# Kernel tuning notes

Measured on AMD Instinct MI355X. Metric: run time of the kernel, lower is better.

Reference implementation:

```python
import jax, jax.numpy as jnp
import numpy as np

B, N, M, C = 1024, 2048, 128, 512
EPS = 1e-8


def setup_inputs() -> dict:
    key = jax.random.key(0)
    k1, k2, k3, k4, k5 = jax.random.split(key, 5)
    x = jax.random.normal(k1, (B, C), dtype=jnp.float32)
    u = jax.random.uniform(k2, (B, N), dtype=jnp.float32) + 1e-3
    w_prev = u / jnp.sum(u, axis=1, keepdims=True)  # valid attention distribution
    mem = jax.random.normal(k3, (B, N, M), dtype=jnp.float32)
    # xavier-uniform-ish fc_read weight (gain 1.4), tiny-std bias
    limit = 1.4 * np.sqrt(6.0 / (C + (M + 6)))
    W = jax.random.uniform(k4, (M + 6, C), dtype=jnp.float32, minval=-limit, maxval=limit)
    b = 0.01 * jax.random.normal(k5, (M + 6,), dtype=jnp.float32)
    return {"x": x, "w_prev": w_prev, "mem": mem, "W": W, "b": b}


def reference(x, w_prev, mem, W, b):
    m = mem.shape[-1]
    o = x @ W.T + b                                   # [B, M+6]
    k = o[:, :m]                                      # key [B, M]
    beta = jax.nn.softplus(o[:, m:m + 1])             # [B, 1]
    g = jax.nn.sigmoid(o[:, m + 1:m + 2])             # [B, 1]
    s = jax.nn.softmax(o[:, m + 2:m + 5], axis=1)     # [B, 3] shift weights
    gamma = 1.0 + jax.nn.softplus(o[:, m + 5:m + 6])  # [B, 1]

    # content addressing: cosine similarity, beta-sharpened softmax
    dot = jnp.einsum('bnm,bm->bn', mem, k)
    denom = jnp.linalg.norm(mem, axis=-1) * jnp.linalg.norm(k, axis=-1, keepdims=True) + EPS
    w_c = jax.nn.softmax(beta * (dot / denom), axis=1)  # [B, N]

    # gate interpolation
    w_g = g * w_c + (1.0 - g) * w_prev

    # circular convolution with 3-tap shift: w_t[i] = sum_j s[j] * w_g[(i+j-1) mod N]
    w_t = (s[:, 0:1] * jnp.roll(w_g, 1, axis=1)
           + s[:, 1:2] * w_g
           + s[:, 2:3] * jnp.roll(w_g, -1, axis=1))

    # sharpening
    w_pow = w_t ** gamma
    w = w_pow / (jnp.sum(w_pow, axis=1, keepdims=True) + 1e-16)

    # weighted read
    r = jnp.einsum('bn,bnm->bm', w, mem)
    return (r, w)
```

## Files before the change

kernel.cpp:

```cpp
#include <hip/hip_runtime.h>
#include <math.h>

#define B 1024
#define N 2048
#define M 128
#define C 512
#define OD (M + 6)
#define EPSF 1e-8f
#define CHUNK 512
#define NCHUNK 4
#define NGRP 64
#define ITERS (B / NGRP)
#define GRID_F (NCHUNK * NGRP)
#define AGENT __HIP_MEMORY_SCOPE_AGENT

__device__ __forceinline__ float softplusf(float x) {
    return fmaxf(x, 0.f) + log1pf(expf(-fabsf(x)));
}
__device__ __forceinline__ float sigmoidf_(float x) {
    return 1.f / (1.f + expf(-x));
}

__device__ __forceinline__ void bar_lds() {
    asm volatile("s_waitcnt lgkmcnt(0)" ::: "memory");
    __builtin_amdgcn_s_barrier();
}

__global__ __launch_bounds__(256) void k_head(
    const float* __restrict__ x, const float* __restrict__ W,
    const float* __restrict__ bias, float* __restrict__ kbuf,
    float* __restrict__ params)
{
    const int b = blockIdx.x;
    __shared__ float xs[C];
    __shared__ float os[OD];
    __shared__ float red[128];

    for (int i = threadIdx.x; i < C; i += 256) xs[i] = x[(size_t)b * C + i];
    __syncthreads();

    if (threadIdx.x < OD) {
        const int j = threadIdx.x;
        const float4* wr = (const float4*)(W + (size_t)j * C);
        float acc = 0.f;
#pragma unroll 8
        for (int c = 0; c < C / 4; ++c) {
            float4 wv = wr[c];
            acc = fmaf(wv.x, xs[4 * c + 0], acc);
            acc = fmaf(wv.y, xs[4 * c + 1], acc);
            acc = fmaf(wv.z, xs[4 * c + 2], acc);
            acc = fmaf(wv.w, xs[4 * c + 3], acc);
        }
        os[j] = acc + bias[j];
    }
    __syncthreads();

    if (threadIdx.x < M) {
        float v = os[threadIdx.x];
        kbuf[(size_t)b * M + threadIdx.x] = v;
        red[threadIdx.x] = v * v;
    }
    __syncthreads();
    for (int s = 64; s > 0; s >>= 1) {
        if (threadIdx.x < s) red[threadIdx.x] += red[threadIdx.x + s];
        __syncthreads();
    }
    if (threadIdx.x == 0) {
        float kn = sqrtf(red[0]);
        float beta = softplusf(os[M]);
        float g = sigmoidf_(os[M + 1]);
        float a0 = os[M + 2], a1 = os[M + 3], a2 = os[M + 4];
        float mx = fmaxf(a0, fmaxf(a1, a2));
        float e0 = expf(a0 - mx), e1 = expf(a1 - mx), e2 = expf(a2 - mx);
        float inv = 1.f / (e0 + e1 + e2);
        float gamma = 1.f + softplusf(os[M + 5]);
        float* p = params + (size_t)b * 8;
        p[0] = beta; p[1] = g; p[2] = e0 * inv; p[3] = e1 * inv;
        p[4] = e2 * inv; p[5] = gamma; p[6] = kn; p[7] = 0.f;
    }
}

__global__ __launch_bounds__(1024, 4) void k_fused(
    const float* __restrict__ mem, const float* __restrict__ kbuf,
    const float* __restrict__ params, const float* __restrict__ w_prev,
    float* __restrict__ w_out,
    float* __restrict__ sPart, float* __restrict__ tPart,
    int* __restrict__ cnt1, float* __restrict__ edgeE,
    float* __restrict__ rpart)
{
    __shared__ float2 redT[CHUNK * 33];
    __shared__ float eA[CHUNK];
    __shared__ float wgA[CHUNK + 2];
    __shared__ float pwA[CHUNK];
    __shared__ float redA[16 * 128];
    __shared__ float partS[16];
    __shared__ float partT[8];
    __shared__ float bcast[4];

    const int tid  = threadIdx.x;
    const int lane = tid & 63;
    const int wv   = tid >> 6;
    const int half = lane >> 5;
    const int l32  = lane & 31;
    const int hw   = wv * 2 + half;

    const int cid  = blockIdx.x >> 6;
    const int bgrp = blockIdx.x & 63;

    for (int it = 0; it < ITERS; ++it) {
        const int b = bgrp * ITERS + it;
        const float* cb = mem + ((size_t)b * N + cid * CHUNK) * M;

        float4 frag[16];
#pragma unroll
        for (int j = 0; j < 16; ++j)
            frag[j] = ((const float4*)(cb + (size_t)(hw * 16 + j) * M))[l32];

        float wp_t = 0.f, wpL = 0.f, wpR = 0.f;
        if (tid < CHUNK)
            wp_t = w_prev[(size_t)b * N + cid * CHUNK + tid];
        if (tid == 0) {
            wpL = w_prev[(size_t)b * N + ((cid * CHUNK + N - 1) & (N - 1))];
            wpR = w_prev[(size_t)b * N + ((cid * CHUNK + CHUNK) & (N - 1))];
        }
        const float4 kv = ((const float4*)(kbuf + (size_t)b * M))[l32];
        const float4 p0 = ((const float4*)(params + (size_t)b * 8))[0];
        const float4 p1 = ((const float4*)(params + (size_t)b * 8))[1];
        const float beta = p0.x, kn = p1.z;

#pragma unroll
        for (int j = 0; j < 16; ++j) {
            const float4 f = frag[j];
            const float dot = f.x * kv.x + f.y * kv.y + f.z * kv.z + f.w * kv.w;
            const float sq  = f.x * f.x + f.y * f.y + f.z * f.z + f.w * f.w;
            redT[(hw * 16 + j) * 33 + l32] = make_float2(dot, sq);
        }
        bar_lds();

        {
            const int r = tid >> 1, q = tid & 1;
            const float2* rowp = &redT[r * 33 + q * 16];
            float dot = 0.f, sq = 0.f;
#pragma unroll
            for (int g = 0; g < 16; ++g) { dot += rowp[g].x; sq += rowp[g].y; }
            dot += __shfl_xor(dot, 1, 64);
            sq  += __shfl_xor(sq,  1, 64);
            float e = 0.f;
            if (q == 0) {
                const float z = beta * dot / (sqrtf(sq) * kn + EPSF);
                e = expf(z);
                eA[r] = e;
            }
            float myS = e;
#pragma unroll
            for (int s = 1; s <= 32; s <<= 1) myS += __shfl_xor(myS, s, 64);
            if (lane == 0) partS[wv] = myS;
        }
        bar_lds();

        if (tid == 0) {
            float S = 0.f;
#pragma unroll
            for (int h = 0; h < 16; ++h) S += partS[h];
            __hip_atomic_store(&sPart[(size_t)b * NCHUNK + cid], S, __ATOMIC_RELAXED, AGENT);
            __hip_atomic_store(&edgeE[((size_t)b * NCHUNK + cid) * 2 + 0], eA[0], __ATOMIC_RELAXED, AGENT);
            __hip_atomic_store(&edgeE[((size_t)b * NCHUNK + cid) * 2 + 1], eA[CHUNK - 1], __ATOMIC_RELAXED, AGENT);
            asm volatile("s_waitcnt vmcnt(0)" ::: "memory");
            __hip_atomic_fetch_add(&cnt1[b], 1, __ATOMIC_RELAXED, AGENT);
            int tries = 0;
            while (__hip_atomic_load(&cnt1[b], __ATOMIC_RELAXED, AGENT) < NCHUNK) {
                __builtin_amdgcn_s_sleep(1);
                if (++tries > (1 << 22)) break;
            }
            float St = 0.f;
#pragma unroll
            for (int c2 = 0; c2 < NCHUNK; ++c2)
                St += __hip_atomic_load(&sPart[(size_t)b * NCHUNK + c2], __ATOMIC_RELAXED, AGENT);
            bcast[0] = 1.f / St;
            bcast[1] = __hip_atomic_load(&edgeE[((size_t)b * NCHUNK + ((cid + NCHUNK - 1) & (NCHUNK - 1))) * 2 + 1], __ATOMIC_RELAXED, AGENT);
            bcast[2] = __hip_atomic_load(&edgeE[((size_t)b * NCHUNK + ((cid + 1) & (NCHUNK - 1))) * 2 + 0], __ATOMIC_RELAXED, AGENT);
        }
        bar_lds();

        const float invS = bcast[0], eL = bcast[1], eR = bcast[2];
        const float g = p0.y, s0p = p0.z, s1p = p0.w, s2p = p1.x, gamma = p1.y;
        if (tid < CHUNK)
            wgA[tid + 1] = g * eA[tid] * invS + (1.f - g) * wp_t;
        if (tid == 0) {
            wgA[0]         = g * eL * invS + (1.f - g) * wpL;
            wgA[CHUNK + 1] = g * eR * invS + (1.f - g) * wpR;
        }
        bar_lds();

        float myT = 0.f;
        if (tid < CHUNK) {
            const float wt = s0p * wgA[tid] + s1p * wgA[tid + 1] + s2p * wgA[tid + 2];
            const float pw = powf(wt, gamma);
            pwA[tid] = pw;
            myT = pw;
        }
#pragma unroll
        for (int s = 32; s >= 1; s >>= 1) myT += __shfl_xor(myT, s, 64);
        if (lane == 0 && wv < 8) partT[wv] = myT;
        bar_lds();

        if (tid == 0) {
            float T = 0.f;
#pragma unroll
            for (int w2 = 0; w2 < 8; ++w2) T += partT[w2];
            tPart[(size_t)b * NCHUNK + cid] = T;
        }

        float4 pwv[4];
#pragma unroll
        for (int q4 = 0; q4 < 4; ++q4)
            pwv[q4] = ((const float4*)&pwA[hw * 16])[q4];
        float4 acc = make_float4(0.f, 0.f, 0.f, 0.f);
#pragma unroll
        for (int j = 0; j < 16; ++j) {
            const float pw = ((const float*)&pwv[j >> 2])[j & 3];
            acc.x = fmaf(pw, frag[j].x, acc.x);
            acc.y = fmaf(pw, frag[j].y, acc.y);
            acc.z = fmaf(pw, frag[j].z, acc.z);
            acc.w = fmaf(pw, frag[j].w, acc.w);
        }
        acc.x += __shfl_xor(acc.x, 32, 64);
        acc.y += __shfl_xor(acc.y, 32, 64);
        acc.z += __shfl_xor(acc.z, 32, 64);
        acc.w += __shfl_xor(acc.w, 32, 64);
        if (half == 0) *(float4*)&redA[wv * 128 + l32 * 4] = acc;
        bar_lds();

        if (tid < 128) {
            float s = 0.f;
#pragma unroll
            for (int w2 = 0; w2 < 16; ++w2) s += redA[w2 * 128 + tid];
            rpart[((size_t)b * NCHUNK + cid) * 128 + tid] = s;
        }
        if (tid < CHUNK)
            w_out[(size_t)b * N + cid * CHUNK + tid] = pwA[tid];
        bar_lds();
    }
}

__global__ __launch_bounds__(256) void k_norm(
    const float* __restrict__ tPart, const float* __restrict__ rpart,
    float* __restrict__ w_out, float* __restrict__ r_out)
{
    const int b = blockIdx.x, tid = threadIdx.x;
    float T = 0.f;
#pragma unroll
    for (int c = 0; c < NCHUNK; ++c) T += tPart[(size_t)b * NCHUNK + c];
    const float invT = 1.f / (T + 1e-16f);

    float4* w4 = (float4*)(w_out + (size_t)b * N);
#pragma unroll
    for (int k = 0; k < 2; ++k) {
        float4 v = w4[tid + k * 256];
        v.x *= invT; v.y *= invT; v.z *= invT; v.w *= invT;
        w4[tid + k * 256] = v;
    }
    if (tid < 128) {
        float s = 0.f;
#pragma unroll
        for (int c = 0; c < NCHUNK; ++c)
            s += rpart[((size_t)b * NCHUNK + c) * 128 + tid];
        r_out[(size_t)b * M + tid] = s * invT;
    }
}

extern "C" void kernel_launch(void* const* d_in, const int* in_sizes, int n_in,
                              void* d_out, int out_size, void* d_ws, size_t ws_size,
                              hipStream_t stream) {
    const float* x      = (const float*)d_in[0];
    const float* w_prev = (const float*)d_in[1];
    const float* mem    = (const float*)d_in[2];
    const float* W      = (const float*)d_in[3];
    const float* bias   = (const float*)d_in[4];

    float* r_out = (float*)d_out;
    float* w_out = (float*)d_out + (size_t)B * M;

    float* ws     = (float*)d_ws;
    float* kbuf   = ws;
    float* params = kbuf + (size_t)B * M;
    float* sPart  = params + (size_t)B * 8;
    float* tPart  = sPart + (size_t)B * NCHUNK;
    int*   cnt1   = (int*)(tPart + (size_t)B * NCHUNK);
    float* edgeE  = (float*)(cnt1 + B);
    float* rpart  = edgeE + (size_t)B * NCHUNK * 2;

    hipMemsetAsync(cnt1, 0, B * sizeof(int), stream);

    k_head<<<B, 256, 0, stream>>>(x, W, bias, kbuf, params);
    k_fused<<<GRID_F, 1024, 0, stream>>>(mem, kbuf, params, w_prev, w_out,
                                         sPart, tPart, cnt1, edgeE, rpart);
    k_norm<<<B, 256, 0, stream>>>(tPart, rpart, w_out, r_out);
}
```

Before: 299.4 us.

## Halve chunk size to double fused blocks and raise occupancy

Splits each batch row's N dimension into 8 chunks of 256 instead of 4 of 512, doubling the fused grid and halving the per-thread memory fragment registers. The launch bound is raised so two 1024-thread blocks can share a CU, keeping more loads in flight for this bandwidth-bound read of mem. The first reduction now pre-combines across half-waves with shuffles, which shrinks the LDS transpose buffer. The cost is more cross-block spin synchronisation per row (8 participants) and the requirement that all 512 blocks be co-resident, which a register spill or LDS overflow would break.

After: 348.6 us. +16.4%, slower.

```diff
diff --git a/kernel.cpp b/kernel.cpp
--- a/kernel.cpp
+++ b/kernel.cpp
@@ -7,8 +7,8 @@
 #define C 512
 #define OD (M + 6)
 #define EPSF 1e-8f
-#define CHUNK 512
-#define NCHUNK 4
+#define CHUNK 256
+#define NCHUNK 8
 #define NGRP 64
 #define ITERS (B / NGRP)
 #define GRID_F (NCHUNK * NGRP)
@@ -80,7 +80,7 @@
     }
 }
 
-__global__ __launch_bounds__(1024, 4) void k_fused(
+__global__ __launch_bounds__(1024, 8) void k_fused(
     const float* __restrict__ mem, const float* __restrict__ kbuf,
     const float* __restrict__ params, const float* __restrict__ w_prev,
     float* __restrict__ w_out,
@@ -88,13 +88,13 @@
     int* __restrict__ cnt1, float* __restrict__ edgeE,
     float* __restrict__ rpart)
 {
-    __shared__ float2 redT[CHUNK * 33];
+    __shared__ float2 redT[CHUNK * 17];
     __shared__ float eA[CHUNK];
     __shared__ float wgA[CHUNK + 2];
     __shared__ float pwA[CHUNK];
     __shared__ float redA[16 * 128];
-    __shared__ float partS[16];
-    __shared__ float partT[8];
+    __shared__ float partS[4];
+    __shared__ float partT[4];
     __shared__ float bcast[4];
 
     const int tid  = threadIdx.x;
@@ -111,10 +111,10 @@
         const int b = bgrp * ITERS + it;
         const float* cb = mem + ((size_t)b * N + cid * CHUNK) * M;
 
-        float4 frag[16];
-#pragma unroll
-        for (int j = 0; j < 16; ++j)
-            frag[j] = ((const float4*)(cb + (size_t)(hw * 16 + j) * M))[l32];
+        float4 frag[8];
+#pragma unroll
+        for (int j = 0; j < 8; ++j)
+            frag[j] = ((const float4*)(cb + (size_t)(hw * 8 + j) * M))[l32];
 
         float wp_t = 0.f, wpL = 0.f, wpR = 0.f;
         if (tid < CHUNK)
@@ -129,39 +129,37 @@
         const float beta = p0.x, kn = p1.z;
 
 #pragma unroll
-        for (int j = 0; j < 16; ++j) {
+        for (int j = 0; j < 8; ++j) {
             const float4 f = frag[j];
-            const float dot = f.x * kv.x + f.y * kv.y + f.z * kv.z + f.w * kv.w;
-            const float sq  = f.x * f.x + f.y * f.y + f.z * f.z + f.w * f.w;
-            redT[(hw * 16 + j) * 33 + l32] = make_float2(dot, sq);
+            float dt = f.x * kv.x + f.y * kv.y + f.z * kv.z + f.w * kv.w;
+            float sq = f.x * f.x + f.y * f.y + f.z * f.z + f.w * f.w;
+            dt += __shfl_xor(dt, 16, 64);
+            sq += __shfl_xor(sq, 16, 64);
+            if (l32 < 16)
+                redT[(hw * 8 + j) * 17 + l32] = make_float2(dt, sq);
         }
         bar_lds();
 
         {
-            const int r = tid >> 1, q = tid & 1;
-            const float2* rowp = &redT[r * 33 + q * 16];
-            float dot = 0.f, sq = 0.f;
-#pragma unroll
-            for (int g = 0; g < 16; ++g) { dot += rowp[g].x; sq += rowp[g].y; }
-            dot += __shfl_xor(dot, 1, 64);
-            sq  += __shfl_xor(sq,  1, 64);
             float e = 0.f;
-            if (q == 0) {
-                const float z = beta * dot / (sqrtf(sq) * kn + EPSF);
+            if (tid < CHUNK) {
+                const float2* rowp = &redT[tid * 17];
+                float dt = 0.f, sq = 0.f;
+#pragma unroll
+                for (int g2 = 0; g2 < 16; ++g2) { dt += rowp[g2].x; sq += rowp[g2].y; }
+                const float z = beta * dt / (sqrtf(sq) * kn + EPSF);
                 e = expf(z);
-                eA[r] = e;
+                eA[tid] = e;
             }
             float myS = e;
 #pragma unroll
-            for (int s = 1; s <= 32; s <<= 1) myS += __shfl_xor(myS, s, 64);
-            if (lane == 0) partS[wv] = myS;
+            for (int s = 32; s >= 1; s >>= 1) myS += __shfl_xor(myS, s, 64);
+            if (lane == 0 && wv < 4) partS[wv] = myS;
         }
         bar_lds();
 
         if (tid == 0) {
-            float S = 0.f;
-#pragma unroll
-            for (int h = 0; h < 16; ++h) S += partS[h];
+            const float S = partS[0] + partS[1] + partS[2] + partS[3];
             __hip_atomic_store(&sPart[(size_t)b * NCHUNK + cid], S, __ATOMIC_RELAXED, AGENT);
             __hip_atomic_store(&edgeE[((size_t)b * NCHUNK + cid) * 2 + 0], eA[0], __ATOMIC_RELAXED, AGENT);
             __hip_atomic_store(&edgeE[((size_t)b * NCHUNK + cid) * 2 + 1], eA[CHUNK - 1], __ATOMIC_RELAXED, AGENT);
@@ -201,34 +199,32 @@
         }
 #pragma unroll
         for (int s = 32; s >= 1; s >>= 1) myT += __shfl_xor(myT, s, 64);
-        if (lane == 0 && wv < 8) partT[wv] = myT;
-        bar_lds();
-
-        if (tid == 0) {
-            float T = 0.f;
-#pragma unroll
-            for (int w2 = 0; w2 < 8; ++w2) T += partT[w2];
-            tPart[(size_t)b * NCHUNK + cid] = T;
-        }
-
-        float4 pwv[4];
-#pragma unroll
-        for (int q4 = 0; q4 < 4; ++q4)
-            pwv[q4] = ((const float4*)&pwA[hw * 16])[q4];
-        float4 acc = make_float4(0.f, 0.f, 0.f, 0.f);
-#pragma unroll
-        for (int j = 0; j < 16; ++j) {
-            const float pw = ((const float*)&pwv[j >> 2])[j & 3];
-            acc.x = fmaf(pw, frag[j].x, acc.x);
-            acc.y = fmaf(pw, frag[j].y, acc.y);
-            acc.z = fmaf(pw, frag[j].z, acc.z);
-            acc.w = fmaf(pw, frag[j].w, acc.w);
-        }
-        acc.x += __shfl_xor(acc.x, 32, 64);
-        acc.y += __shfl_xor(acc.y, 32, 64);
-        acc.z += __shfl_xor(acc.z, 32, 64);
-        acc.w += __shfl_xor(acc.w, 32, 64);
-        if (half == 0) *(float4*)&redA[wv * 128 + l32 * 4] = acc;
+        if (lane == 0 && wv < 4) partT[wv] = myT;
+        bar_lds();
+
+        if (tid == 0)
+            tPart[(size_t)b * NCHUNK + cid] = partT[0] + partT[1] + partT[2] + partT[3];
+
+        {
+            float4 pwv[2];
+#pragma unroll
+            for (int q4 = 0; q4 < 2; ++q4)
+                pwv[q4] = ((const float4*)&pwA[hw * 8])[q4];
+            float4 acc = make_float4(0.f, 0.f, 0.f, 0.f);
+#pragma unroll
+            for (int j = 0; j < 8; ++j) {
+                const float pw = ((const float*)&pwv[j >> 2])[j & 3];
+                acc.x = fmaf(pw, frag[j].x, acc.x);
+                acc.y = fmaf(pw, frag[j].y, acc.y);
+                acc.z = fmaf(pw, frag[j].z, acc.z);
+                acc.w = fmaf(pw, frag[j].w, acc.w);
+            }
+            acc.x += __shfl_xor(acc.x, 32, 64);
+            acc.y += __shfl_xor(acc.y, 32, 64);
+            acc.z += __shfl_xor(acc.z, 32, 64);
+            acc.w += __shfl_xor(acc.w, 32, 64);
+            if (half == 0) *(float4*)&redA[wv * 128 + l32 * 4] = acc;
+        }
         bar_lds();
 
         if (tid < 128) {
```
